# Optimization experiments

Measured on AMD Instinct MI355X. Metric: run time of the kernel, lower is better.

The kernel has to match this reference:

```python
import jax, jax.numpy as jnp
import numpy as np

N_NODES = 50000
N_EDGES = 1000000
N_GRAPHS = 64
IN_FEATS, HIDDEN, N_CLASSES = 64, 64, 32


def setup_inputs() -> dict:
    key = jax.random.key(0)
    ks = jax.random.split(key, 10)
    x = jax.random.normal(ks[0], (N_NODES, IN_FEATS), dtype=jnp.float32)
    eh = jax.random.normal(ks[1], (N_EDGES,), dtype=jnp.float32)
    src = jax.random.randint(ks[2], (N_EDGES,), 0, N_NODES)
    dst = jax.random.randint(ks[3], (N_EDGES,), 0, N_NODES)
    node_graph = jnp.sort(jax.random.randint(ks[4], (N_NODES,), 0, N_GRAPHS))
    # GraphConv parameters (glorot-ish scale)
    W1 = jax.random.normal(ks[5], (IN_FEATS, HIDDEN), dtype=jnp.float32) / np.sqrt(IN_FEATS)
    b1 = jnp.zeros((HIDDEN,), dtype=jnp.float32)
    W2 = jax.random.normal(ks[6], (HIDDEN, N_CLASSES), dtype=jnp.float32) / np.sqrt(HIDDEN)
    b2 = jnp.zeros((N_CLASSES,), dtype=jnp.float32)
    mu = jnp.array(0.0, dtype=jnp.float32)
    # sigma = -1.0 keeps log((eh-mu)^2 / -sigma) in a valid domain (module default 1.0 -> NaN)
    sigma = jnp.array(-1.0, dtype=jnp.float32)
    return {"x": x, "eh": eh, "src": src, "dst": dst, "node_graph": node_graph,
            "W1": W1, "b1": b1, "W2": W2, "b2": b2, "mu": mu, "sigma": sigma}


def _graph_conv(x, W, b, src, dst, ew, norm_src, norm_dst):
    # DGL GraphConv(norm='both') with per-edge scalar weight ew:
    # h = D_in^{-1/2} * A_w * (D_out^{-1/2} * x) @ W + b
    xs = x * norm_src  # [N, F]
    msg = xs[src] * ew[:, None]  # gather + edge-weight multiply  [E, F]
    agg = jax.ops.segment_sum(msg, dst, num_segments=x.shape[0])  # scatter-add [N, F]
    return (agg * norm_dst) @ W + b


def reference(x, eh, src, dst, node_graph, W1, b1, W2, b2, mu, sigma):
    n = x.shape[0]
    ones_e = jnp.ones_like(eh)
    deg_out = jnp.clip(jax.ops.segment_sum(ones_e, src, num_segments=n), 1.0)
    deg_in = jnp.clip(jax.ops.segment_sum(ones_e, dst, num_segments=n), 1.0)
    norm_src = jax.lax.rsqrt(deg_out)[:, None]  # [N,1]
    norm_dst = jax.lax.rsqrt(deg_in)[:, None]   # [N,1]

    # edge feature transform: log((h - mu)^2 / -sigma)
    d = eh - mu
    efeat = jnp.log(d * d / -sigma)  # [E]

    h = _graph_conv(x, W1, b1, src, dst, efeat, norm_src, norm_dst)
    h = jax.nn.relu(h)
    h = _graph_conv(h, W2, b2, src, dst, efeat, norm_src, norm_dst)

    # dgl.mean_nodes: per-graph mean over nodes
    g_sum = jax.ops.segment_sum(h, node_graph, num_segments=N_GRAPHS)  # [B, C]
    g_cnt = jnp.clip(jax.ops.segment_sum(jnp.ones((n,), jnp.float32), node_graph,
                                         num_segments=N_GRAPHS), 1.0)
    return g_sum / g_cnt[:, None]
```

## Files before the change

kernel.cpp:

```cpp
#include <hip/hip_runtime.h>

#define NGRAPHS 64
#define NCLS 32
#define G1 256

__device__ inline unsigned bfpack(float lo, float hi) {
    unsigned ulo = __float_as_uint(lo); ulo += 0x7fffu + ((ulo >> 16) & 1u);
    unsigned uhi = __float_as_uint(hi); uhi += 0x7fffu + ((uhi >> 16) & 1u);
    return (ulo >> 16) | (uhi & 0xffff0000u);
}
__device__ inline float bflo(unsigned p) { return __uint_as_float(p << 16); }
__device__ inline float bfhi(unsigned p) { return __uint_as_float(p & 0xffff0000u); }
__device__ inline float bfs(unsigned short u) { return __uint_as_float((unsigned)u << 16); }

__global__ __launch_bounds__(256) void part_hist_scatter(
    const float* __restrict__ eh, const int* __restrict__ src,
    const int* __restrict__ dst, const float* __restrict__ mu,
    const float* __restrict__ sigma, int* __restrict__ gHd,
    int* __restrict__ gHs, int* __restrict__ gLocD, int* __restrict__ gLocS,
    int2* __restrict__ partD, unsigned char* __restrict__ partS, int nE) {
    __shared__ int hd[256], hs[256], tmp[256], locD[256], locS[256];
    int t = threadIdx.x, blk = blockIdx.x;
    hd[t] = 0; hs[t] = 0;
    __syncthreads();
    int chunk = (nE + G1 - 1) / G1;
    int beg = blk * chunk, end = min(beg + chunk, nE);
    for (int i = beg + t; i < end; i += 256) {
        atomicAdd(&hd[((unsigned)dst[i]) >> 8], 1);
        atomicAdd(&hs[((unsigned)src[i]) >> 8], 1);
    }
    __syncthreads();
    gHd[t * G1 + blk] = hd[t];
    gHs[t * G1 + blk] = hs[t];
    tmp[t] = hd[t];
    __syncthreads();
    for (int o = 1; o < 256; o <<= 1) {
        int u = (t >= o) ? tmp[t - o] : 0;
        __syncthreads();
        tmp[t] += u;
        __syncthreads();
    }
    locD[t] = tmp[t] - hd[t];
    gLocD[blk * 256 + t] = locD[t];
    __syncthreads();
    tmp[t] = hs[t];
    __syncthreads();
    for (int o = 1; o < 256; o <<= 1) {
        int u = (t >= o) ? tmp[t - o] : 0;
        __syncthreads();
        tmp[t] += u;
        __syncthreads();
    }
    locS[t] = tmp[t] - hs[t];
    gLocS[blk * 256 + t] = locS[t];
    hd[t] = 0; hs[t] = 0;
    __syncthreads();
    float mu0 = mu[0], inv = -1.f / sigma[0];
    size_t wbase = (size_t)blk * chunk;
    for (int i = beg + t; i < end; i += 256) {
        int d = dst[i], s = src[i];
        float df = eh[i] - mu0;
        float w = logf(df * df * inv);
        int bu = ((unsigned)d) >> 8;
        int r = atomicAdd(&hd[bu], 1);
        partD[wbase + locD[bu] + r] = make_int2((s << 8) | (d & 255), __float_as_int(w));
        int bs = ((unsigned)s) >> 8;
        int r2 = atomicAdd(&hs[bs], 1);
        partS[wbase + locS[bs] + r2] = (unsigned char)(s & 255);
    }
}

__global__ __launch_bounds__(1024) void part_scan(int* __restrict__ a, int* __restrict__ b) {
    __shared__ int part[1024];
    int* arr = blockIdx.x ? b : a;
    int t = threadIdx.x;
    int base = t * 64;
    int v[64], s = 0;
#pragma unroll
    for (int j = 0; j < 64; ++j) { v[j] = arr[base + j]; s += v[j]; }
    part[t] = s;
    __syncthreads();
    for (int o = 1; o < 1024; o <<= 1) {
        int u = (t >= o) ? part[t - o] : 0;
        __syncthreads();
        part[t] += u;
        __syncthreads();
    }
    int run = part[t] - s;
#pragma unroll
    for (int j = 0; j < 64; ++j) { arr[base + j] = run; run += v[j]; }
    if (t == 1023) arr[65536] = run;
}

__global__ __launch_bounds__(256) void bucket_build(const int2* __restrict__ partD,
    const unsigned char* __restrict__ partS, const int* __restrict__ gHd,
    const int* __restrict__ gHs, const int* __restrict__ gLocD,
    const int* __restrict__ gLocS, int* __restrict__ csr_src,
    unsigned short* __restrict__ csr_w, int* __restrict__ row_start,
    float* __restrict__ norm_dst, float* __restrict__ norm_src, int nN, int nE) {
    __shared__ int deg[256], loff[256], cnt[256];
    int b = blockIdx.x, t = threadIdx.x;
    int chunk = (nE + G1 - 1) / G1;
    int begD = gHd[b * G1];
    int lenD = gHd[b * G1 + t + 1] - gHd[b * G1 + t];
    size_t offD = (size_t)t * chunk + gLocD[t * 256 + b];
    deg[t] = 0; cnt[t] = 0;
    __syncthreads();
    for (int i = 0; i < lenD; i += 4) {
        int lo4[4];
#pragma unroll
        for (int u = 0; u < 4; ++u)
            lo4[u] = partD[offD + min(i + u, lenD - 1)].x & 255;
#pragma unroll
        for (int u = 0; u < 4; ++u)
            if (i + u < lenD) atomicAdd(&deg[lo4[u]], 1);
    }
    __syncthreads();
    loff[t] = deg[t];
    __syncthreads();
    for (int o = 1; o < 256; o <<= 1) {
        int u = (t >= o) ? loff[t - o] : 0;
        __syncthreads();
        loff[t] += u;
        __syncthreads();
    }
    loff[t] -= deg[t];
    __syncthreads();
    int n = b * 256 + t;
    if (n < nN) {
        row_start[n] = begD + loff[t];
        norm_dst[n] = rsqrtf((float)max(deg[t], 1));
    }
    if (b == 0 && t == 0) row_start[nN] = nE;
    for (int i = 0; i < lenD; i += 4) {
        int2 r4[4];
#pragma unroll
        for (int u = 0; u < 4; ++u)
            r4[u] = partD[offD + min(i + u, lenD - 1)];
#pragma unroll
        for (int u = 0; u < 4; ++u) {
            if (i + u < lenD) {
                int lo = r4[u].x & 255;
                int pos = atomicAdd(&cnt[lo], 1);
                int idx = begD + loff[lo] + pos;
                csr_src[idx] = r4[u].x >> 8;
                unsigned uw = (unsigned)r4[u].y;
                csr_w[idx] = (unsigned short)((uw + 0x7fffu + ((uw >> 16) & 1u)) >> 16);
            }
        }
    }
    __syncthreads();
    deg[t] = 0;
    __syncthreads();
    int lenS = gHs[b * G1 + t + 1] - gHs[b * G1 + t];
    size_t offS = (size_t)t * chunk + gLocS[t * 256 + b];
    for (int i = 0; i < lenS; i += 8) {
        int v8[8];
#pragma unroll
        for (int u = 0; u < 8; ++u)
            v8[u] = partS[offS + min(i + u, lenS - 1)];
#pragma unroll
        for (int u = 0; u < 8; ++u)
            if (i + u < lenS) atomicAdd(&deg[v8[u]], 1);
    }
    __syncthreads();
    if (n < nN) norm_src[n] = rsqrtf((float)max(deg[t], 1));
}

__global__ __launch_bounds__(256) void xw_mm(const float* __restrict__ x,
    const float* __restrict__ norm_src, const float* __restrict__ W1,
    unsigned* __restrict__ xw, int nN) {
    __shared__ float sW[64 * 64];
    __shared__ float srow[4][64];
    int t = threadIdx.x;
    for (int i = t; i < 64 * 64; i += 256) sW[i] = W1[i];
    __syncthreads();
    int wid = t >> 6, k = t & 63;
    int base = blockIdx.x * 32;
    for (int it = 0; it < 8; ++it) {
        int n = base + it * 4 + wid;
        if (n >= nN) break;
        srow[wid][k] = x[((size_t)n << 6) + k] * norm_src[n];
        float acc0 = 0.f, acc1 = 0.f;
#pragma unroll
        for (int i = 0; i < 64; i += 2) {
            acc0 += srow[wid][i] * sW[i * 64 + k];
            acc1 += srow[wid][i + 1] * sW[(i + 1) * 64 + k];
        }
        float outv = acc0 + acc1;
        float other = __shfl_xor(outv, 1, 64);
        if ((k & 1) == 0) xw[((size_t)n << 5) + (k >> 1)] = bfpack(outv, other);
    }
}

#define LCSR(P, bg, en) { \
    int last_ = max((en) - 1, 0); \
    _Pragma("unroll") \
    for (int u = 0; u < 6; ++u) { \
        int sl = (bg) + q + 4 * u; \
        int slc = (sl < (en)) ? sl : last_; \
        P##s[u] = csr_src[slc]; \
        float wv = bfs(csr_w[slc]); \
        P##w[u] = (sl < (en)) ? wv : 0.f; \
    } }
#define LGAT(P) { \
    _Pragma("unroll") \
    for (int u = 0; u < 6; ++u) P##p[u] = xw2[((size_t)P##s[u] << 4) + j]; }
#define LFMA(P) { \
    _Pragma("unroll") \
    for (int u = 0; u < 6; ++u) { \
        a0 += P##w[u] * bflo(P##p[u].x); a1 += P##w[u] * bfhi(P##p[u].x); \
        a2 += P##w[u] * bflo(P##p[u].y); a3 += P##w[u] * bfhi(P##p[u].y); } }
#define REM(P, bg, en) { \
    for (int sl0 = (bg) + q + 24; sl0 < (en); sl0 += 24) { \
        int last_ = (en) - 1; \
        _Pragma("unroll") \
        for (int u = 0; u < 6; ++u) { \
            int sl = sl0 + 4 * u; \
            int slc = (sl < (en)) ? sl : last_; \
            P##s[u] = csr_src[slc]; \
            float wv = bfs(csr_w[slc]); \
            P##w[u] = (sl < (en)) ? wv : 0.f; } \
        _Pragma("unroll") \
        for (int u = 0; u < 6; ++u) P##p[u] = xw2[((size_t)P##s[u] << 4) + j]; \
        LFMA(P) } }
#define EPI(nd_, ns_, n_) { \
    a0 += __shfl_xor(a0, 16, 64); a0 += __shfl_xor(a0, 32, 64); \
    a1 += __shfl_xor(a1, 16, 64); a1 += __shfl_xor(a1, 32, 64); \
    a2 += __shfl_xor(a2, 16, 64); a2 += __shfl_xor(a2, 32, 64); \
    a3 += __shfl_xor(a3, 16, 64); a3 += __shfl_xor(a3, 32, 64); \
    if (q == 0) { \
        float4 v; \
        v.x = fmaxf(a0 * (nd_) + bv.x, 0.f) * (ns_); \
        v.y = fmaxf(a1 * (nd_) + bv.y, 0.f) * (ns_); \
        v.z = fmaxf(a2 * (nd_) + bv.z, 0.f) * (ns_); \
        v.w = fmaxf(a3 * (nd_) + bv.w, 0.f) * (ns_); \
        *reinterpret_cast<float4*>(&srow[wid][4 * j]) = v; } \
    { int jj = lane & 31, ib = lane & 32; \
      float c0 = 0.f, c1 = 0.f; \
      _Pragma("unroll") \
      for (int i = 0; i < 32; i += 2) { \
          c0 += srow[wid][ib + i] * sW[(ib + i) * NCLS + jj]; \
          c1 += srow[wid][ib + i + 1] * sW[(ib + i + 1) * NCLS + jj]; } \
      float part = c0 + c1; \
      part += __shfl_xor(part, 32, 64); \
      float other = __shfl_xor(part, 1, 64); \
      if (ib == 0 && (jj & 1) == 0 && (n_) < nN) \
          hw[((size_t)(n_) << 4) + (jj >> 1)] = bfpack(part, other); } }

__global__ __launch_bounds__(256) void gather1_mm(const unsigned* __restrict__ xw,
    const int* __restrict__ row_start, const int* __restrict__ csr_src,
    const unsigned short* __restrict__ csr_w, const float* __restrict__ norm_dst,
    const float* __restrict__ norm_src, const float* __restrict__ W2f,
    const float* __restrict__ b1, unsigned* __restrict__ hw, int nN) {
    __shared__ float sW[64 * NCLS];
    __shared__ float srow[4][64];
    __shared__ int rs[17];
    int t = threadIdx.x;
    int base = blockIdx.x * 16;
    for (int i = t; i < 64 * NCLS; i += 256) sW[i] = W2f[i];
    if (t < 17) rs[t] = row_start[min(base + t, nN)];
    __syncthreads();
    int wid = t >> 6, lane = t & 63;
    int q = lane >> 4, j = lane & 15;
    const uint2* xw2 = reinterpret_cast<const uint2*>(xw);
    float4 bv = reinterpret_cast<const float4*>(b1)[j];
    int n0 = base + wid, n1 = n0 + 4, n2 = n0 + 8, n3 = n0 + 12;
    int nc = nN - 1;
    float nd0 = norm_dst[min(n0, nc)], ns0 = norm_src[min(n0, nc)];
    float nd1 = norm_dst[min(n1, nc)], ns1 = norm_src[min(n1, nc)];
    float nd2 = norm_dst[min(n2, nc)], ns2 = norm_src[min(n2, nc)];
    float nd3 = norm_dst[min(n3, nc)], ns3 = norm_src[min(n3, nc)];
    int r0b = __builtin_amdgcn_readfirstlane(rs[wid]);
    int r0e = __builtin_amdgcn_readfirstlane(rs[wid + 1]);
    int r1b = __builtin_amdgcn_readfirstlane(rs[wid + 4]);
    int r1e = __builtin_amdgcn_readfirstlane(rs[wid + 5]);
    int r2b = __builtin_amdgcn_readfirstlane(rs[wid + 8]);
    int r2e = __builtin_amdgcn_readfirstlane(rs[wid + 9]);
    int r3b = __builtin_amdgcn_readfirstlane(rs[wid + 12]);
    int r3e = __builtin_amdgcn_readfirstlane(rs[wid + 13]);
    int As[6]; float Aw[6]; uint2 Ap[6];
    int Bs[6]; float Bw[6]; uint2 Bp[6];
    float a0, a1, a2, a3;
    LCSR(A, r0b, r0e)
    LGAT(A)
    LCSR(B, r1b, r1e)
    LGAT(B)
    a0 = a1 = a2 = a3 = 0.f;
    LFMA(A)
    REM(A, r0b, r0e)
    LCSR(A, r2b, r2e)
    EPI(nd0, ns0, n0)
    LGAT(A)
    a0 = a1 = a2 = a3 = 0.f;
    LFMA(B)
    REM(B, r1b, r1e)
    LCSR(B, r3b, r3e)
    EPI(nd1, ns1, n1)
    LGAT(B)
    a0 = a1 = a2 = a3 = 0.f;
    LFMA(A)
    REM(A, r2b, r2e)
    EPI(nd2, ns2, n2)
    a0 = a1 = a2 = a3 = 0.f;
    LFMA(B)
    REM(B, r3b, r3e)
    EPI(nd3, ns3, n3)
}

#define LCSR2(P, bg, en) { \
    int last_ = max((en) - 1, 0); \
    _Pragma("unroll") \
    for (int u = 0; u < 2; ++u) { \
        int sl = (bg) + o + 8 * u; \
        int slc = (sl < (en)) ? sl : last_; \
        P##s[u] = csr_src[slc]; \
        float wv = bfs(csr_w[slc]); \
        P##w[u] = (sl < (en)) ? wv : 0.f; \
    } }
#define LGAT2(P) { \
    _Pragma("unroll") \
    for (int u = 0; u < 2; ++u) P##p[u] = hw2[((size_t)P##s[u] << 3) + j]; }
#define LFMA2(P) { \
    _Pragma("unroll") \
    for (int u = 0; u < 2; ++u) { \
        a0 += P##w[u] * bflo(P##p[u].x); a1 += P##w[u] * bfhi(P##p[u].x); \
        a2 += P##w[u] * bflo(P##p[u].y); a3 += P##w[u] * bfhi(P##p[u].y); } }
#define REM2(P, bg, en) { \
    for (int sl0 = (bg) + o + 16; sl0 < (en); sl0 += 16) { \
        int last_ = (en) - 1; \
        _Pragma("unroll") \
        for (int u = 0; u < 2; ++u) { \
            int sl = sl0 + 8 * u; \
            int slc = (sl < (en)) ? sl : last_; \
            P##s[u] = csr_src[slc]; \
            float wv = bfs(csr_w[slc]); \
            P##w[u] = (sl < (en)) ? wv : 0.f; } \
        _Pragma("unroll") \
        for (int u = 0; u < 2; ++u) P##p[u] = hw2[((size_t)P##s[u] << 3) + j]; \
        LFMA2(P) } }
#define EPI2(nd_, n_) { \
    a0 += __shfl_xor(a0, 8, 64); a0 += __shfl_xor(a0, 16, 64); a0 += __shfl_xor(a0, 32, 64); \
    a1 += __shfl_xor(a1, 8, 64); a1 += __shfl_xor(a1, 16, 64); a1 += __shfl_xor(a1, 32, 64); \
    a2 += __shfl_xor(a2, 8, 64); a2 += __shfl_xor(a2, 16, 64); a2 += __shfl_xor(a2, 32, 64); \
    a3 += __shfl_xor(a3, 8, 64); a3 += __shfl_xor(a3, 16, 64); a3 += __shfl_xor(a3, 32, 64); \
    if (lane < 8 && (n_) < nN) { \
        uint2 outv; \
        outv.x = bfpack(a0 * (nd_), a1 * (nd_)); \
        outv.y = bfpack(a2 * (nd_), a3 * (nd_)); \
        reinterpret_cast<uint2*>(agg2)[((size_t)(n_) << 3) + j] = outv; } }

__global__ __launch_bounds__(256) void gather2(const unsigned* __restrict__ hw,
    const int* __restrict__ row_start, const int* __restrict__ csr_src,
    const unsigned short* __restrict__ csr_w, const float* __restrict__ norm_dst,
    unsigned* __restrict__ agg2, int nN) {
    __shared__ int rs[17];
    int t = threadIdx.x;
    int base = blockIdx.x * 16;
    if (t < 17) rs[t] = row_start[min(base + t, nN)];
    __syncthreads();
    int wid = t >> 6, lane = t & 63;
    int o = lane >> 3, j = lane & 7;
    const uint2* hw2 = reinterpret_cast<const uint2*>(hw);
    int n0 = base + wid, n1 = n0 + 4, n2 = n0 + 8, n3 = n0 + 12;
    int nc = nN - 1;
    float nd0 = norm_dst[min(n0, nc)], nd1 = norm_dst[min(n1, nc)];
    float nd2 = norm_dst[min(n2, nc)], nd3 = norm_dst[min(n3, nc)];
    int r0b = __builtin_amdgcn_readfirstlane(rs[wid]);
    int r0e = __builtin_amdgcn_readfirstlane(rs[wid + 1]);
    int r1b = __builtin_amdgcn_readfirstlane(rs[wid + 4]);
    int r1e = __builtin_amdgcn_readfirstlane(rs[wid + 5]);
    int r2b = __builtin_amdgcn_readfirstlane(rs[wid + 8]);
    int r2e = __builtin_amdgcn_readfirstlane(rs[wid + 9]);
    int r3b = __builtin_amdgcn_readfirstlane(rs[wid + 12]);
    int r3e = __builtin_amdgcn_readfirstlane(rs[wid + 13]);
    int As[2]; float Aw[2]; uint2 Ap[2];
    int Bs[2]; float Bw[2]; uint2 Bp[2];
    float a0, a1, a2, a3;
    LCSR2(A, r0b, r0e)
    LGAT2(A)
    LCSR2(B, r1b, r1e)
    LGAT2(B)
    a0 = a1 = a2 = a3 = 0.f;
    LFMA2(A)
    REM2(A, r0b, r0e)
    LCSR2(A, r2b, r2e)
    EPI2(nd0, n0)
    LGAT2(A)
    a0 = a1 = a2 = a3 = 0.f;
    LFMA2(B)
    REM2(B, r1b, r1e)
    LCSR2(B, r3b, r3e)
    EPI2(nd1, n1)
    LGAT2(B)
    a0 = a1 = a2 = a3 = 0.f;
    LFMA2(A)
    REM2(A, r2b, r2e)
    EPI2(nd2, n2)
    a0 = a1 = a2 = a3 = 0.f;
    LFMA2(B)
    REM2(B, r3b, r3e)
    EPI2(nd3, n3)
}

__global__ __launch_bounds__(256) void pool_out(const unsigned* __restrict__ agg2,
    const int* __restrict__ ng, const float* __restrict__ b2,
    float* __restrict__ out, int nN) {
    __shared__ float gacc[NCLS];
    int g = blockIdx.x, t = threadIdx.x;
    if (t < NCLS) gacc[t] = 0.f;
    __syncthreads();
    int lo = 0, hi = nN;
    while (lo < hi) { int m = (lo + hi) >> 1; if (ng[m] < g) lo = m + 1; else hi = m; }
    int lb = lo;
    lo = 0; hi = nN;
    while (lo < hi) { int m = (lo + hi) >> 1; if (ng[m] < g + 1) lo = m + 1; else hi = m; }
    int ub = lo;
    int r = t >> 4, j = t & 15;
    float ax = 0.f, ay = 0.f;
    for (int n = lb + r; n < ub; n += 16) {
        unsigned p = agg2[((size_t)n << 4) + j];
        ax += bflo(p); ay += bfhi(p);
    }
    atomicAdd(&gacc[2 * j], ax);
    atomicAdd(&gacc[2 * j + 1], ay);
    __syncthreads();
    if (t < NCLS) {
        float cnt = (float)(ub - lb);
        out[g * NCLS + t] = (gacc[t] + b2[t] * cnt) / fmaxf(cnt, 1.f);
    }
}

extern "C" void kernel_launch(void* const* d_in, const int* in_sizes, int n_in,
                              void* d_out, int out_size, void* d_ws, size_t ws_size,
                              hipStream_t stream) {
    const float* x   = (const float*)d_in[0];
    const float* eh  = (const float*)d_in[1];
    const int*   src = (const int*)d_in[2];
    const int*   dst = (const int*)d_in[3];
    const int*   ng  = (const int*)d_in[4];
    const float* W1  = (const float*)d_in[5];
    const float* b1  = (const float*)d_in[6];
    const float* W2  = (const float*)d_in[7];
    const float* b2  = (const float*)d_in[8];
    const float* mu  = (const float*)d_in[9];
    const float* sg  = (const float*)d_in[10];
    const int nN = in_sizes[0] / 64;
    const int nE = in_sizes[1];
    const int NBUK = (nN + 255) / 256;
    const int chunk = (nE + G1 - 1) / G1;

    char* wsb = (char*)d_ws;
    int* gHd = (int*)wsb;
    int* gHs = gHd + 65537;
    int* gLocD = gHs + 65537;
    int* gLocS = gLocD + 65536;
    int* row_start = gLocS + 65536;
    float* norm_src = (float*)(row_start + nN + 1);
    float* norm_dst = norm_src + nN;
    size_t off = (size_t)((char*)(norm_dst + nN) - wsb);
    off = (off + 15) & ~(size_t)15;
    int2* partD = (int2*)(wsb + off);
    unsigned char* partS = (unsigned char*)(partD + (size_t)G1 * chunk);
    off = (size_t)((char*)(partS + (size_t)G1 * chunk) - wsb);
    off = (off + 15) & ~(size_t)15;
    int* csr_src = (int*)(wsb + off);
    unsigned short* csr_w = (unsigned short*)(csr_src + nE);
    off = (size_t)((char*)(csr_w + nE) - wsb);
    off = (off + 15) & ~(size_t)15;
    unsigned* xw   = (unsigned*)(wsb + off);
    unsigned* hw   = xw + (size_t)nN * 32;
    unsigned* agg2 = hw + (size_t)nN * 16;

    part_hist_scatter<<<G1, 256, 0, stream>>>(eh, src, dst, mu, sg, gHd, gHs,
                                              gLocD, gLocS, partD, partS, nE);
    part_scan<<<2, 1024, 0, stream>>>(gHd, gHs);
    bucket_build<<<NBUK, 256, 0, stream>>>(partD, partS, gHd, gHs, gLocD, gLocS,
                                           csr_src, csr_w, row_start,
                                           norm_dst, norm_src, nN, nE);
    xw_mm<<<(nN + 31) / 32, 256, 0, stream>>>(x, norm_src, W1, xw, nN);
    gather1_mm<<<(nN + 15) / 16, 256, 0, stream>>>(xw, row_start, csr_src, csr_w,
                                                   norm_dst, norm_src, W2, b1, hw, nN);
    gather2<<<(nN + 15) / 16, 256, 0, stream>>>(hw, row_start, csr_src, csr_w,
                                                norm_dst, agg2, nN);
    pool_out<<<NGRAPHS, 256, 0, stream>>>(agg2, ng, b2, (float*)d_out, nN);

    (void)n_in; (void)out_size; (void)ws_size;
}
```

Measured before the change: 165.4 us.

## Fuse mean-node pooling into second gather via shared-memory atomics and last-block finalize

The per-graph mean pooling kernel is removed. The second aggregation kernel now accumulates its results directly into a shared per-graph accumulator, flushes the nonzero entries to a global buffer with atomics, and uses a ticket counter so the last block computes the final means. This drops the bf16 agg2 intermediate write and read plus one launch. In exchange each block clears and scans an 8KB shared array and issues global atomics, and a separate change unrolls the edge loop three-wide instead of two.

```diff
diff --git a/kernel.cpp b/kernel.cpp
--- a/kernel.cpp
+++ b/kernel.cpp
@@ -70,10 +70,15 @@
     }
 }
 
-__global__ __launch_bounds__(1024) void part_scan(int* __restrict__ a, int* __restrict__ b) {
+__global__ __launch_bounds__(1024) void part_scan(int* __restrict__ a,
+    int* __restrict__ b, float* __restrict__ gout, int* __restrict__ done) {
     __shared__ int part[1024];
+    int t = threadIdx.x;
+    if (blockIdx.x == 0) {
+        gout[t] = 0.f; gout[t + 1024] = 0.f;
+        if (t == 0) *done = 0;
+    }
     int* arr = blockIdx.x ? b : a;
-    int t = threadIdx.x;
     int base = t * 64;
     int v[64], s = 0;
 #pragma unroll
@@ -311,7 +316,7 @@
 #define LCSR2(P, bg, en) { \
     int last_ = max((en) - 1, 0); \
     _Pragma("unroll") \
-    for (int u = 0; u < 2; ++u) { \
+    for (int u = 0; u < 3; ++u) { \
         int sl = (bg) + o + 8 * u; \
         int slc = (sl < (en)) ? sl : last_; \
         P##s[u] = csr_src[slc]; \
@@ -320,43 +325,49 @@
     } }
 #define LGAT2(P) { \
     _Pragma("unroll") \
-    for (int u = 0; u < 2; ++u) P##p[u] = hw2[((size_t)P##s[u] << 3) + j]; }
+    for (int u = 0; u < 3; ++u) P##p[u] = hw2[((size_t)P##s[u] << 3) + j]; }
 #define LFMA2(P) { \
     _Pragma("unroll") \
-    for (int u = 0; u < 2; ++u) { \
+    for (int u = 0; u < 3; ++u) { \
         a0 += P##w[u] * bflo(P##p[u].x); a1 += P##w[u] * bfhi(P##p[u].x); \
         a2 += P##w[u] * bflo(P##p[u].y); a3 += P##w[u] * bfhi(P##p[u].y); } }
 #define REM2(P, bg, en) { \
-    for (int sl0 = (bg) + o + 16; sl0 < (en); sl0 += 16) { \
+    for (int sl0 = (bg) + o + 24; sl0 < (en); sl0 += 24) { \
         int last_ = (en) - 1; \
         _Pragma("unroll") \
-        for (int u = 0; u < 2; ++u) { \
+        for (int u = 0; u < 3; ++u) { \
             int sl = sl0 + 8 * u; \
             int slc = (sl < (en)) ? sl : last_; \
             P##s[u] = csr_src[slc]; \
             float wv = bfs(csr_w[slc]); \
             P##w[u] = (sl < (en)) ? wv : 0.f; } \
         _Pragma("unroll") \
-        for (int u = 0; u < 2; ++u) P##p[u] = hw2[((size_t)P##s[u] << 3) + j]; \
+        for (int u = 0; u < 3; ++u) P##p[u] = hw2[((size_t)P##s[u] << 3) + j]; \
         LFMA2(P) } }
-#define EPI2(nd_, n_) { \
+#define EPI2(nd_, g_, n_) { \
     a0 += __shfl_xor(a0, 8, 64); a0 += __shfl_xor(a0, 16, 64); a0 += __shfl_xor(a0, 32, 64); \
     a1 += __shfl_xor(a1, 8, 64); a1 += __shfl_xor(a1, 16, 64); a1 += __shfl_xor(a1, 32, 64); \
     a2 += __shfl_xor(a2, 8, 64); a2 += __shfl_xor(a2, 16, 64); a2 += __shfl_xor(a2, 32, 64); \
     a3 += __shfl_xor(a3, 8, 64); a3 += __shfl_xor(a3, 16, 64); a3 += __shfl_xor(a3, 32, 64); \
     if (lane < 8 && (n_) < nN) { \
-        uint2 outv; \
-        outv.x = bfpack(a0 * (nd_), a1 * (nd_)); \
-        outv.y = bfpack(a2 * (nd_), a3 * (nd_)); \
-        reinterpret_cast<uint2*>(agg2)[((size_t)(n_) << 3) + j] = outv; } }
-
-__global__ __launch_bounds__(256) void gather2(const unsigned* __restrict__ hw,
+        atomicAdd(&gacc[(g_) * NCLS + 4 * j + 0], a0 * (nd_)); \
+        atomicAdd(&gacc[(g_) * NCLS + 4 * j + 1], a1 * (nd_)); \
+        atomicAdd(&gacc[(g_) * NCLS + 4 * j + 2], a2 * (nd_)); \
+        atomicAdd(&gacc[(g_) * NCLS + 4 * j + 3], a3 * (nd_)); } }
+
+__global__ __launch_bounds__(256) void gather2_pool(const unsigned* __restrict__ hw,
     const int* __restrict__ row_start, const int* __restrict__ csr_src,
     const unsigned short* __restrict__ csr_w, const float* __restrict__ norm_dst,
-    unsigned* __restrict__ agg2, int nN) {
+    const int* __restrict__ ng, const float* __restrict__ b2,
+    float* __restrict__ gout, int* __restrict__ done,
+    float* __restrict__ out, int nN) {
+    __shared__ float gacc[NGRAPHS * NCLS];
     __shared__ int rs[17];
+    __shared__ int ticket;
+    __shared__ int cnts[NGRAPHS];
     int t = threadIdx.x;
     int base = blockIdx.x * 16;
+    for (int i = t; i < NGRAPHS * NCLS; i += 256) gacc[i] = 0.f;
     if (t < 17) rs[t] = row_start[min(base + t, nN)];
     __syncthreads();
     int wid = t >> 6, lane = t & 63;
@@ -366,6 +377,8 @@
     int nc = nN - 1;
     float nd0 = norm_dst[min(n0, nc)], nd1 = norm_dst[min(n1, nc)];
     float nd2 = norm_dst[min(n2, nc)], nd3 = norm_dst[min(n3, nc)];
+    int g0 = ng[min(n0, nc)], g1 = ng[min(n1, nc)];
+    int g2 = ng[min(n2, nc)], g3 = ng[min(n3, nc)];
     int r0b = __builtin_amdgcn_readfirstlane(rs[wid]);
     int r0e = __builtin_amdgcn_readfirstlane(rs[wid + 1]);
     int r1b = __builtin_amdgcn_readfirstlane(rs[wid + 4]);
@@ -374,8 +387,8 @@
     int r2e = __builtin_amdgcn_readfirstlane(rs[wid + 9]);
     int r3b = __builtin_amdgcn_readfirstlane(rs[wid + 12]);
     int r3e = __builtin_amdgcn_readfirstlane(rs[wid + 13]);
-    int As[2]; float Aw[2]; uint2 Ap[2];
-    int Bs[2]; float Bw[2]; uint2 Bp[2];
+    int As[3]; float Aw[3]; uint2 Ap[3];
+    int Bs[3]; float Bw[3]; uint2 Bp[3];
     float a0, a1, a2, a3;
     LCSR2(A, r0b, r0e)
     LGAT2(A)
@@ -385,49 +398,47 @@
     LFMA2(A)
     REM2(A, r0b, r0e)
     LCSR2(A, r2b, r2e)
-    EPI2(nd0, n0)
+    EPI2(nd0, g0, n0)
     LGAT2(A)
     a0 = a1 = a2 = a3 = 0.f;
     LFMA2(B)
     REM2(B, r1b, r1e)
     LCSR2(B, r3b, r3e)
-    EPI2(nd1, n1)
+    EPI2(nd1, g1, n1)
     LGAT2(B)
     a0 = a1 = a2 = a3 = 0.f;
     LFMA2(A)
     REM2(A, r2b, r2e)
-    EPI2(nd2, n2)
+    EPI2(nd2, g2, n2)
     a0 = a1 = a2 = a3 = 0.f;
     LFMA2(B)
     REM2(B, r3b, r3e)
-    EPI2(nd3, n3)
-}
-
-__global__ __launch_bounds__(256) void pool_out(const unsigned* __restrict__ agg2,
-    const int* __restrict__ ng, const float* __restrict__ b2,
-    float* __restrict__ out, int nN) {
-    __shared__ float gacc[NCLS];
-    int g = blockIdx.x, t = threadIdx.x;
-    if (t < NCLS) gacc[t] = 0.f;
-    __syncthreads();
-    int lo = 0, hi = nN;
-    while (lo < hi) { int m = (lo + hi) >> 1; if (ng[m] < g) lo = m + 1; else hi = m; }
-    int lb = lo;
-    lo = 0; hi = nN;
-    while (lo < hi) { int m = (lo + hi) >> 1; if (ng[m] < g + 1) lo = m + 1; else hi = m; }
-    int ub = lo;
-    int r = t >> 4, j = t & 15;
-    float ax = 0.f, ay = 0.f;
-    for (int n = lb + r; n < ub; n += 16) {
-        unsigned p = agg2[((size_t)n << 4) + j];
-        ax += bflo(p); ay += bfhi(p);
-    }
-    atomicAdd(&gacc[2 * j], ax);
-    atomicAdd(&gacc[2 * j + 1], ay);
-    __syncthreads();
-    if (t < NCLS) {
-        float cnt = (float)(ub - lb);
-        out[g * NCLS + t] = (gacc[t] + b2[t] * cnt) / fmaxf(cnt, 1.f);
+    EPI2(nd3, g3, n3)
+    __syncthreads();
+    for (int i = t; i < NGRAPHS * NCLS; i += 256) {
+        float v = gacc[i];
+        if (v != 0.f) atomicAdd(&gout[i], v);
+    }
+    __threadfence();
+    if (t == 0) ticket = atomicAdd(done, 1);
+    __syncthreads();
+    if (ticket == (int)gridDim.x - 1) {
+        if (t < NGRAPHS) {
+            int g = t;
+            int lo = 0, hi = nN;
+            while (lo < hi) { int m = (lo + hi) >> 1; if (ng[m] < g) lo = m + 1; else hi = m; }
+            int lb = lo;
+            lo = 0; hi = nN;
+            while (lo < hi) { int m = (lo + hi) >> 1; if (ng[m] < g + 1) lo = m + 1; else hi = m; }
+            cnts[g] = lo - lb;
+        }
+        __syncthreads();
+        for (int i = t; i < NGRAPHS * NCLS; i += 256) {
+            int g = i >> 5, f = i & 31;
+            float cnt = (float)cnts[g];
+            float sum = atomicAdd(&gout[i], 0.f);
+            out[i] = (sum + b2[f] * cnt) / fmaxf(cnt, 1.f);
+        }
     }
 }
 
@@ -458,7 +469,9 @@
     int* row_start = gLocS + 65536;
     float* norm_src = (float*)(row_start + nN + 1);
     float* norm_dst = norm_src + nN;
-    size_t off = (size_t)((char*)(norm_dst + nN) - wsb);
+    float* gout = norm_dst + nN;
+    int* done = (int*)(gout + NGRAPHS * NCLS);
+    size_t off = (size_t)((char*)(done + 1) - wsb);
     off = (off + 15) & ~(size_t)15;
     int2* partD = (int2*)(wsb + off);
     unsigned char* partS = (unsigned char*)(partD + (size_t)G1 * chunk);
@@ -470,20 +483,19 @@
     off = (off + 15) & ~(size_t)15;
     unsigned* xw   = (unsigned*)(wsb + off);
     unsigned* hw   = xw + (size_t)nN * 32;
-    unsigned* agg2 = hw + (size_t)nN * 16;
 
     part_hist_scatter<<<G1, 256, 0, stream>>>(eh, src, dst, mu, sg, gHd, gHs,
                                               gLocD, gLocS, partD, partS, nE);
-    part_scan<<<2, 1024, 0, stream>>>(gHd, gHs);
+    part_scan<<<2, 1024, 0, stream>>>(gHd, gHs, gout, done);
     bucket_build<<<NBUK, 256, 0, stream>>>(partD, partS, gHd, gHs, gLocD, gLocS,
                                            csr_src, csr_w, row_start,
                                            norm_dst, norm_src, nN, nE);
     xw_mm<<<(nN + 31) / 32, 256, 0, stream>>>(x, norm_src, W1, xw, nN);
     gather1_mm<<<(nN + 15) / 16, 256, 0, stream>>>(xw, row_start, csr_src, csr_w,
                                                    norm_dst, norm_src, W2, b1, hw, nN);
-    gather2<<<(nN + 15) / 16, 256, 0, stream>>>(hw, row_start, csr_src, csr_w,
-                                                norm_dst, agg2, nN);
-    pool_out<<<NGRAPHS, 256, 0, stream>>>(agg2, ng, b2, (float*)d_out, nN);
+    gather2_pool<<<(nN + 15) / 16, 256, 0, stream>>>(hw, row_start, csr_src, csr_w,
+                                                     norm_dst, ng, b2, gout, done,
+                                                     (float*)d_out, nN);
 
     (void)n_in; (void)out_size; (void)ws_size;
 }
```

Measured after the change: 362.2 us. 119% more time.
